# Kernel tuning notes

Measured on AMD Instinct MI355X. Metric: run time of the kernel, lower is better.

## Reference

```python
import jax, jax.numpy as jnp
import numpy as np
import math

B, T, S, C, H = 2, 2048, 576, 1024, 16
D = C // H
EPS = 1e-5


def _ln(x, w, b):
    m = jnp.mean(x, axis=-1, keepdims=True)
    v = jnp.mean((x - m) ** 2, axis=-1, keepdims=True)
    return (x - m) * jax.lax.rsqrt(v + EPS) * w + b


def setup_inputs() -> dict:
    key = jax.random.key(0)
    ks = jax.random.split(key, 20)
    s = 0.02
    return {
        "x": jax.random.normal(ks[0], (B, T, C), jnp.float32),
        "context": jax.random.normal(ks[1], (B, S, C), jnp.float32),
        "ln1_w": jnp.ones((C,), jnp.float32), "ln1_b": jnp.zeros((C,), jnp.float32),
        "ln2_w": jnp.ones((C,), jnp.float32), "ln2_b": jnp.zeros((C,), jnp.float32),
        "ln3_w": jnp.ones((C,), jnp.float32), "ln3_b": jnp.zeros((C,), jnp.float32),
        "attn_wqkv": jax.random.normal(ks[2], (C, 3 * C), jnp.float32) * s,
        "attn_bqkv": jnp.zeros((3 * C,), jnp.float32),
        "attn_wproj": jax.random.normal(ks[3], (C, C), jnp.float32) * s,
        "attn_bproj": jnp.zeros((C,), jnp.float32),
        "ca_wq": jax.random.normal(ks[4], (C, C), jnp.float32) * s,
        "ca_bq": jnp.zeros((C,), jnp.float32),
        "ca_wk": jax.random.normal(ks[5], (C, C), jnp.float32) * s,
        "ca_bk": jnp.zeros((C,), jnp.float32),
        "ca_wv": jax.random.normal(ks[6], (C, C), jnp.float32) * s,
        "ca_bv": jnp.zeros((C,), jnp.float32),
        "ca_wproj": jax.random.normal(ks[7], (C, C), jnp.float32) * s,
        "ca_bproj": jnp.zeros((C,), jnp.float32),
        "fc_w": jax.random.normal(ks[8], (C, 4 * C), jnp.float32) * s,
        "fc_b": jnp.zeros((4 * C,), jnp.float32),
        "proj_w": jax.random.normal(ks[9], (4 * C, C), jnp.float32) * s,
        "proj_b": jnp.zeros((C,), jnp.float32),
    }


def reference(x, context, ln1_w, ln1_b, ln2_w, ln2_b, ln3_w, ln3_b,
              attn_wqkv, attn_bqkv, attn_wproj, attn_bproj,
              ca_wq, ca_bq, ca_wk, ca_bk, ca_wv, ca_bv, ca_wproj, ca_bproj,
              fc_w, fc_b, proj_w, proj_b):
    b, t, c = x.shape
    scale = 1.0 / math.sqrt(D)

    # --- causal self-attention ---
    h = _ln(x, ln1_w, ln1_b)
    qkv = h @ attn_wqkv + attn_bqkv                       # [B,T,3C]
    q, k, v = jnp.split(qkv, 3, axis=-1)
    q = q.reshape(b, t, H, D).transpose(0, 2, 1, 3)       # [B,H,T,D]
    k = k.reshape(b, t, H, D).transpose(0, 2, 1, 3)
    v = v.reshape(b, t, H, D).transpose(0, 2, 1, 3)
    att = jnp.einsum('bhqd,bhkd->bhqk', q, k) * scale     # [B,H,T,T]
    causal = jnp.tril(jnp.ones((t, t), dtype=bool))
    att = jnp.where(causal, att, -jnp.inf)
    att = jax.nn.softmax(att, axis=-1)
    sa = jnp.einsum('bhqk,bhkd->bhqd', att, v).transpose(0, 2, 1, 3).reshape(b, t, c)
    x = x + sa @ attn_wproj + attn_bproj

    # --- cross-attention ---
    h = _ln(x, ln2_w, ln2_b)
    s = context.shape[1]
    q = (h @ ca_wq + ca_bq).reshape(b, t, H, D).transpose(0, 2, 1, 3)        # [B,H,T,D]
    k = (context @ ca_wk + ca_bk).reshape(b, s, H, D).transpose(0, 2, 1, 3)  # [B,H,S,D]
    v = (context @ ca_wv + ca_bv).reshape(b, s, H, D).transpose(0, 2, 1, 3)
    scores = jnp.einsum('bhqd,bhkd->bhqk', q, k) * scale                      # [B,H,T,S]
    attn_prob = jax.nn.softmax(scores, axis=-1)
    ca = jnp.einsum('bhqk,bhkd->bhqd', attn_prob, v).transpose(0, 2, 1, 3).reshape(b, t, c)
    x = x + ca @ ca_wproj + ca_bproj

    # --- GELU(tanh) MLP ---
    h = _ln(x, ln3_w, ln3_b)
    h = jax.nn.gelu(h @ fc_w + fc_b, approximate=True)
    x = x + h @ proj_w + proj_b
    return x, attn_prob
```

## Files before the change

kernel.cpp:

```cpp
#include <hip/hip_runtime.h>

typedef __bf16 bf16_t;
typedef __attribute__((ext_vector_type(8))) __bf16 bf16x8;
typedef __attribute__((ext_vector_type(4))) __bf16 bf16x4;
typedef __attribute__((ext_vector_type(4))) float f32x4;

static constexpr int kB = 2, kT = 2048, kS = 576, kC = 1024, kH = 16, kD = 64;

#define MFMA16(a, b, c) __builtin_amdgcn_mfma_f32_16x16x32_bf16((a), (b), (c), 0, 0, 0)

__device__ __forceinline__ void gld_lds16(const bf16_t* g, bf16_t* l) {
    __builtin_amdgcn_global_load_lds((const __attribute__((address_space(1))) unsigned int*)g,
                                     (__attribute__((address_space(3))) unsigned int*)l, 16, 0, 0);
}

__device__ __forceinline__ int swz(int row, int q) { return row * 64 + (((q ^ (row & 7)) & 7) << 3); }

__device__ inline float gelu_tanh(float x) {
    float u = 1.5957691216057308f * (x + 0.044715f * x * x * x);
    float t = 1.f - 2.f / (__expf(u) + 1.f);
    return 0.5f * x * (1.f + t);
}

__global__ void transpose_w(const float* __restrict__ W, bf16_t* __restrict__ WT, int K, int N) {
    __shared__ float tile[32][33];
    int n0 = blockIdx.x * 32, k0 = blockIdx.y * 32;
    int tx = threadIdx.x, ty = threadIdx.y;
#pragma unroll
    for (int i = 0; i < 4; ++i)
        tile[ty + i * 8][tx] = W[(size_t)(k0 + ty + i * 8) * N + n0 + tx];
    __syncthreads();
#pragma unroll
    for (int i = 0; i < 4; ++i)
        WT[(size_t)(n0 + ty + i * 8) * K + k0 + tx] = (bf16_t)tile[tx][ty + i * 8];
}

__global__ void f32_to_bf16(const float* __restrict__ in, bf16_t* __restrict__ out, int n4) {
    int i = blockIdx.x * 256 + threadIdx.x;
    if (i < n4) {
        float4 v = ((const float4*)in)[i];
        bf16x4 o;
        o[0] = (bf16_t)v.x; o[1] = (bf16_t)v.y; o[2] = (bf16_t)v.z; o[3] = (bf16_t)v.w;
        ((bf16x4*)out)[i] = o;
    }
}

__global__ __launch_bounds__(256) void ln_kernel(const float* __restrict__ x,
                                                 const float* __restrict__ w,
                                                 const float* __restrict__ bb,
                                                 bf16_t* __restrict__ out) {
    int row = blockIdx.x, tid = threadIdx.x;
    const float* xr = x + (size_t)row * kC;
    float4 v = ((const float4*)xr)[tid];
    float s1 = v.x + v.y + v.z + v.w;
    float s2 = v.x * v.x + v.y * v.y + v.z * v.z + v.w * v.w;
#pragma unroll
    for (int o = 32; o > 0; o >>= 1) {
        s1 += __shfl_down(s1, o);
        s2 += __shfl_down(s2, o);
    }
    __shared__ float red[8];
    __shared__ float mv[2];
    int wid = tid >> 6, lane = tid & 63;
    if (lane == 0) { red[wid] = s1; red[4 + wid] = s2; }
    __syncthreads();
    if (tid == 0) {
        float a = red[0] + red[1] + red[2] + red[3];
        float c = red[4] + red[5] + red[6] + red[7];
        float mean = a * (1.f / kC);
        float var = c * (1.f / kC) - mean * mean;
        mv[0] = mean;
        mv[1] = rsqrtf(var + 1e-5f);
    }
    __syncthreads();
    float mean = mv[0], rstd = mv[1];
    float4 wv = ((const float4*)w)[tid];
    float4 bv = ((const float4*)bb)[tid];
    bf16x4 o4;
    o4[0] = (bf16_t)((v.x - mean) * rstd * wv.x + bv.x);
    o4[1] = (bf16_t)((v.y - mean) * rstd * wv.y + bv.y);
    o4[2] = (bf16_t)((v.z - mean) * rstd * wv.z + bv.z);
    o4[3] = (bf16_t)((v.w - mean) * rstd * wv.w + bv.w);
    *(bf16x4*)&out[(size_t)row * kC + tid * 4] = o4;
}

#define VWAIT(n) asm volatile("s_waitcnt vmcnt(" #n ")" ::: "memory")
#define CFENCE() asm volatile("" ::: "memory")

template <int EPI, int BM>
__global__ __launch_bounds__(256) void gemm128(const bf16_t* __restrict__ A, const bf16_t* __restrict__ Bw,
                                               const float* __restrict__ bias, const float* __restrict__ res,
                                               void* __restrict__ Out, void* __restrict__ Out2,
                                               void* __restrict__ Out3, int M, int N, int K, int lda, int ldb,
                                               int ldc) {
    constexpr int MT = BM / 32;
    constexpr int ASZ = BM * 64, BSZ = 128 * 64;
    __shared__ __align__(16) bf16_t As[2 * ASZ];
    __shared__ __align__(16) bf16_t Bs[2 * BSZ];
    const int tid = threadIdx.x;
    const int m0 = blockIdx.y * BM, n0 = blockIdx.x * 128;
    const int lane = tid & 63, wid = tid >> 6;
    const int l16 = lane & 15, quad = lane >> 4;
    const int wm = (wid >> 1) * (BM / 2), wn = (wid & 1) * 64;
    f32x4 acc[MT][4] = {};

    const bf16_t* Ab = A + (size_t)m0 * lda;
    const bf16_t* Bb = Bw + (size_t)n0 * ldb;

    auto stage = [&](int buf, int k0) {
#pragma unroll
        for (int i = 0; i < BM / 32; ++i) {
            int chunk = tid + i * 256;
            int row = chunk >> 3, c8 = chunk & 7;
            gld_lds16(Ab + (size_t)row * lda + k0 + ((c8 ^ (row & 7)) << 3), As + buf * ASZ + chunk * 8);
        }
#pragma unroll
        for (int i = 0; i < 4; ++i) {
            int chunk = tid + i * 256;
            int row = chunk >> 3, c8 = chunk & 7;
            gld_lds16(Bb + (size_t)row * ldb + k0 + ((c8 ^ (row & 7)) << 3), Bs + buf * BSZ + chunk * 8);
        }
    };

    const int nk = K / 64;
    stage(0, 0);
    int cur = 0;
    for (int t = 0; t < nk; ++t) {
        __builtin_amdgcn_s_barrier();
        CFENCE();
        if (t + 1 < nk) {
            stage(cur ^ 1, (t + 1) * 64);
            if constexpr (BM == 64) VWAIT(6); else VWAIT(8);
        } else {
            VWAIT(0);
        }
        __builtin_amdgcn_s_barrier();
        CFENCE();
#pragma unroll
        for (int kk = 0; kk < 2; ++kk) {
            bf16x8 af[MT], bw[4];
#pragma unroll
            for (int mt = 0; mt < MT; ++mt)
                af[mt] = *(const bf16x8*)&As[cur * ASZ + swz(wm + mt * 16 + l16, kk * 4 + quad)];
#pragma unroll
            for (int nt = 0; nt < 4; ++nt)
                bw[nt] = *(const bf16x8*)&Bs[cur * BSZ + swz(wn + nt * 16 + l16, kk * 4 + quad)];
#pragma unroll
            for (int mt = 0; mt < MT; ++mt)
#pragma unroll
                for (int nt = 0; nt < 4; ++nt) acc[mt][nt] = MFMA16(af[mt], bw[nt], acc[mt][nt]);
        }
        cur ^= 1;
    }

#pragma unroll
    for (int mt = 0; mt < MT; ++mt)
#pragma unroll
        for (int nt = 0; nt < 4; ++nt) {
            int n = n0 + wn + nt * 16 + l16;
            float bv = bias ? bias[n] : 0.f;
#pragma unroll
            for (int r = 0; r < 4; ++r) {
                int m = m0 + wm + mt * 16 + quad * 4 + r;
                float v = acc[mt][nt][r] + bv;
                if constexpr (EPI == 2) v = gelu_tanh(v);
                if constexpr (EPI == 0 || EPI == 2) {
                    ((bf16_t*)Out)[(size_t)m * ldc + n] = (bf16_t)v;
                } else if constexpr (EPI == 1) {
                    ((float*)Out)[(size_t)m * ldc + n] = v + res[(size_t)m * ldc + n];
                } else {
                    int b = m >> 11, t = m & 2047;
                    if (n < 2048) {
                        int h = (n & 1023) >> 6, d = n & 63;
                        bf16_t* dst = (n < 1024) ? (bf16_t*)Out : (bf16_t*)Out2;
                        dst[(((size_t)b * kH + h) * kT + t) * kD + d] = (bf16_t)v;
                    } else {
                        int n2 = n - 2048;
                        int h = n2 >> 6, d = n2 & 63;
                        ((bf16_t*)Out3)[(((size_t)b * kH + h) * kD + d) * kT + t] = (bf16_t)v;
                    }
                }
            }
        }
}

__global__ __launch_bounds__(256) void flash_self4(const bf16_t* __restrict__ qb, const bf16_t* __restrict__ kb,
                                                   const bf16_t* __restrict__ vT, bf16_t* __restrict__ sa) {
    const int tid = threadIdx.x;
    const int qi = gridDim.x - 1 - blockIdx.x;
    const int h = blockIdx.y, b = blockIdx.z;
    const int lane = tid & 63, wid = tid >> 6;
    const int l16 = lane & 15, quad = lane >> 4;
    const size_t bh = (size_t)b * kH + h;
    constexpr int TSZ = 64 * 64;

    __shared__ __align__(16) bf16_t Qs[TSZ];
    __shared__ __align__(16) bf16_t Ks[2 * TSZ];
    __shared__ __align__(16) bf16_t VTs[2 * TSZ];
    bf16_t* Ps = Qs;

    const bf16_t* qsrc = qb + (bh * kT + (size_t)qi * 64) * kD;
    const bf16_t* kbase = kb + bh * kT * kD;
    const bf16_t* vbase = vT + bh * kD * kT;

#pragma unroll
    for (int i = 0; i < 2; ++i) {
        int chunk = tid + i * 256;
        int row = chunk >> 3, c8 = chunk & 7;
        gld_lds16(qsrc + row * 64 + ((c8 ^ (row & 7)) << 3), Qs + chunk * 8);
    }

    auto stageKV = [&](int buf, int kt) {
        const bf16_t* ksrc = kbase + (size_t)kt * 64 * kD;
        const bf16_t* vsrc = vbase + (size_t)kt * 64;
#pragma unroll
        for (int i = 0; i < 2; ++i) {
            int chunk = tid + i * 256;
            int row = chunk >> 3, c8 = chunk & 7;
            int sc = (c8 ^ (row & 7)) << 3;
            gld_lds16(ksrc + row * 64 + sc, Ks + buf * TSZ + chunk * 8);
            gld_lds16(vsrc + (size_t)row * kT + sc, VTs + buf * TSZ + chunk * 8);
        }
    };
    stageKV(0, 0);

    __syncthreads();
    bf16x8 aq[2];
    aq[0] = *(const bf16x8*)&Qs[swz(wid * 16 + l16, quad)];
    aq[1] = *(const bf16x8*)&Qs[swz(wid * 16 + l16, 4 + quad)];
#pragma unroll
    for (int j = 0; j < 8; ++j) { aq[0][j] *= (bf16_t)0.125f; aq[1][j] *= (bf16_t)0.125f; }

    f32x4 o[4] = {};
    float lsum[4] = {0.f, 0.f, 0.f, 0.f};
    const int qrow = qi * 64 + wid * 16 + quad * 4;
    int cur = 0;

    for (int kt = 0; kt <= qi; ++kt) {
        if (kt) __syncthreads();
        if (kt < qi) stageKV(cur ^ 1, kt + 1);

        f32x4 sf[4] = {};
#pragma unroll
        for (int kk = 0; kk < 2; ++kk)
#pragma unroll
            for (int nt = 0; nt < 4; ++nt) {
                bf16x8 bk = *(const bf16x8*)&Ks[cur * TSZ + swz(nt * 16 + l16, kk * 4 + quad)];
                sf[nt] = MFMA16(aq[kk], bk, sf[nt]);
            }

        const bool diag = (kt == qi);
#pragma unroll
        for (int nt = 0; nt < 4; ++nt) {
            int col = kt * 64 + nt * 16 + l16;
#pragma unroll
            for (int r = 0; r < 4; ++r) {
                float s = sf[nt][r];
                if (diag && col > qrow + r) s = -1e30f;
                float p = __expf(s);
                lsum[r] += p;
                int rp = wid * 16 + quad * 4 + r;
                int cc = nt * 16 + l16;
                Ps[rp * 64 + (cc ^ ((rp & 7) << 3))] = (bf16_t)p;
            }
        }
#pragma unroll
        for (int kk = 0; kk < 2; ++kk) {
            bf16x8 ap = *(const bf16x8*)&Ps[swz(wid * 16 + l16, kk * 4 + quad)];
#pragma unroll
            for (int dt = 0; dt < 4; ++dt) {
                bf16x8 bv = *(const bf16x8*)&VTs[cur * TSZ + swz(dt * 16 + l16, kk * 4 + quad)];
                o[dt] = MFMA16(ap, bv, o[dt]);
            }
        }
        cur ^= 1;
    }

#pragma unroll
    for (int r = 0; r < 4; ++r) {
        float s = lsum[r];
#pragma unroll
        for (int off = 1; off < 16; off <<= 1) s += __shfl_xor(s, off, 16);
        float inv = 1.f / s;
        size_t row = (size_t)b * kT + qi * 64 + wid * 16 + quad * 4 + r;
#pragma unroll
        for (int dt = 0; dt < 4; ++dt)
            sa[row * kC + h * kD + dt * 16 + l16] = (bf16_t)(o[dt][r] * inv);
    }
}

__global__ __launch_bounds__(256) void ca_fused(const bf16_t* __restrict__ q2, const bf16_t* __restrict__ k2,
                                                const bf16_t* __restrict__ v2T, bf16_t* __restrict__ ca,
                                                float* __restrict__ probs) {
    const int tid = threadIdx.x;
    const int qi = blockIdx.x, z = blockIdx.y;
    const int b = z >> 4, h = z & 15;
    const int lane = tid & 63, wid = tid >> 6;
    const int l16 = lane & 15, quad = lane >> 4;
    const size_t bh = (size_t)z;
    constexpr int TSZ = 64 * 64;

    __shared__ __align__(16) bf16_t Qs[TSZ];
    __shared__ __align__(16) bf16_t Ks[2 * TSZ];
    __shared__ __align__(16) bf16_t VTs[2 * TSZ];
    bf16_t* Ps = Qs;

#pragma unroll
    for (int i = 0; i < 2; ++i) {
        int chunk = tid + i * 256;
        int row = chunk >> 3, c8 = chunk & 7;
        gld_lds16(q2 + ((size_t)(b * kT + qi * 64 + row)) * kC + h * kD + ((c8 ^ (row & 7)) << 3),
                  Qs + chunk * 8);
    }

    auto stageKV = [&](int buf, int kt) {
#pragma unroll
        for (int i = 0; i < 2; ++i) {
            int chunk = tid + i * 256;
            int row = chunk >> 3, c8 = chunk & 7;
            int sc = (c8 ^ (row & 7)) << 3;
            gld_lds16(k2 + ((size_t)(b * kS + kt * 64 + row)) * kC + h * kD + sc, Ks + buf * TSZ + chunk * 8);
            gld_lds16(v2T + (bh * kD + row) * kS + kt * 64 + sc, VTs + buf * TSZ + chunk * 8);
        }
    };
    stageKV(0, 0);

    __syncthreads();
    bf16x8 aq[2];
    aq[0] = *(const bf16x8*)&Qs[swz(wid * 16 + l16, quad)];
    aq[1] = *(const bf16x8*)&Qs[swz(wid * 16 + l16, 4 + quad)];
#pragma unroll
    for (int j = 0; j < 8; ++j) { aq[0][j] *= (bf16_t)0.125f; aq[1][j] *= (bf16_t)0.125f; }

    f32x4 o[4] = {};
    float lsum[4] = {0.f, 0.f, 0.f, 0.f};
    bf16x4 pk[9][4];
    int cur = 0;

#pragma unroll
    for (int kt = 0; kt < 9; ++kt) {
        if (kt) __syncthreads();
        if (kt < 8) stageKV(cur ^ 1, kt + 1);

        f32x4 sf[4] = {};
#pragma unroll
        for (int kk = 0; kk < 2; ++kk)
#pragma unroll
            for (int nt = 0; nt < 4; ++nt) {
                bf16x8 bk = *(const bf16x8*)&Ks[cur * TSZ + swz(nt * 16 + l16, kk * 4 + quad)];
                sf[nt] = MFMA16(aq[kk], bk, sf[nt]);
            }
#pragma unroll
        for (int nt = 0; nt < 4; ++nt) {
            bf16x4 pc;
#pragma unroll
            for (int r = 0; r < 4; ++r) {
                float p = __expf(sf[nt][r]);
                lsum[r] += p;
                bf16_t pb = (bf16_t)p;
                pc[r] = pb;
                int rp = wid * 16 + quad * 4 + r;
                int cc = nt * 16 + l16;
                Ps[rp * 64 + (cc ^ ((rp & 7) << 3))] = pb;
            }
            pk[kt][nt] = pc;
        }
#pragma unroll
        for (int kk = 0; kk < 2; ++kk) {
            bf16x8 ap = *(const bf16x8*)&Ps[swz(wid * 16 + l16, kk * 4 + quad)];
#pragma unroll
            for (int dt = 0; dt < 4; ++dt) {
                bf16x8 bv = *(const bf16x8*)&VTs[cur * TSZ + swz(dt * 16 + l16, kk * 4 + quad)];
                o[dt] = MFMA16(ap, bv, o[dt]);
            }
        }
        cur ^= 1;
    }

    float inv[4];
#pragma unroll
    for (int r = 0; r < 4; ++r) {
        float s = lsum[r];
#pragma unroll
        for (int off = 1; off < 16; off <<= 1) s += __shfl_xor(s, off, 16);
        inv[r] = 1.f / s;
        size_t row = (size_t)b * kT + qi * 64 + wid * 16 + quad * 4 + r;
#pragma unroll
        for (int dt = 0; dt < 4; ++dt)
            ca[row * kC + h * kD + dt * 16 + l16] = (bf16_t)(o[dt][r] * inv[r]);
    }
#pragma unroll
    for (int r = 0; r < 4; ++r) {
        float* dst = probs + ((size_t)z * kT + qi * 64 + wid * 16 + quad * 4 + r) * kS;
#pragma unroll
        for (int kt = 0; kt < 9; ++kt)
#pragma unroll
            for (int nt = 0; nt < 4; ++nt)
                dst[kt * 64 + nt * 16 + l16] = (float)pk[kt][nt][r] * inv[r];
    }
}

__global__ void v_transpose(const bf16_t* __restrict__ v2, bf16_t* __restrict__ v2T) {
    int idx = blockIdx.x * 256 + threadIdx.x;
    int s = idx % kS;
    int t = idx / kS;
    int d = t % kD; t /= kD;
    int h = t % kH;
    int b = t / kH;
    v2T[idx] = v2[((size_t)(b * kS + s)) * kC + h * kD + d];
}

extern "C" void kernel_launch(void* const* d_in, const int* in_sizes, int n_in, void* d_out, int out_size,
                              void* d_ws, size_t ws_size, hipStream_t stream) {
    const float* x = (const float*)d_in[0];
    const float* context = (const float*)d_in[1];
    const float* ln1_w = (const float*)d_in[2];
    const float* ln1_b = (const float*)d_in[3];
    const float* ln2_w = (const float*)d_in[4];
    const float* ln2_b = (const float*)d_in[5];
    const float* ln3_w = (const float*)d_in[6];
    const float* ln3_b = (const float*)d_in[7];
    const float* attn_wqkv = (const float*)d_in[8];
    const float* attn_bqkv = (const float*)d_in[9];
    const float* attn_wproj = (const float*)d_in[10];
    const float* attn_bproj = (const float*)d_in[11];
    const float* ca_wq = (const float*)d_in[12];
    const float* ca_bq = (const float*)d_in[13];
    const float* ca_wk = (const float*)d_in[14];
    const float* ca_bk = (const float*)d_in[15];
    const float* ca_wv = (const float*)d_in[16];
    const float* ca_bv = (const float*)d_in[17];
    const float* ca_wproj = (const float*)d_in[18];
    const float* ca_bproj = (const float*)d_in[19];
    const float* fc_w = (const float*)d_in[20];
    const float* fc_b = (const float*)d_in[21];
    const float* proj_w = (const float*)d_in[22];
    const float* proj_b = (const float*)d_in[23];

    float* out_x = (float*)d_out;
    float* probs = out_x + (size_t)kB * kT * kC;

    char* wsp = (char*)d_ws;
    size_t off = 0;
    auto alloc = [&](size_t bytes) -> void* {
        void* p = wsp + off;
        off += (bytes + 255) & ~(size_t)255;
        return p;
    };
    bf16_t* wT_qkv   = (bf16_t*)alloc((size_t)3 * kC * kC * 2);
    bf16_t* wT_aproj = (bf16_t*)alloc((size_t)kC * kC * 2);
    bf16_t* wT_caq   = (bf16_t*)alloc((size_t)kC * kC * 2);
    bf16_t* wT_cak   = (bf16_t*)alloc((size_t)kC * kC * 2);
    bf16_t* wT_cav   = (bf16_t*)alloc((size_t)kC * kC * 2);
    bf16_t* wT_caproj= (bf16_t*)alloc((size_t)kC * kC * 2);
    bf16_t* wT_fc    = (bf16_t*)alloc((size_t)4 * kC * kC * 2);
    bf16_t* wT_proj  = (bf16_t*)alloc((size_t)4 * kC * kC * 2);
    bf16_t* hbuf     = (bf16_t*)alloc((size_t)kB * kT * kC * 2);
    bf16_t* qb       = (bf16_t*)alloc((size_t)kB * kT * kC * 2);
    bf16_t* kbuf     = (bf16_t*)alloc((size_t)kB * kT * kC * 2);
    bf16_t* vTb      = (bf16_t*)alloc((size_t)kB * kT * kC * 2);
    bf16_t* sabuf    = (bf16_t*)alloc((size_t)kB * kT * kC * 2);
    float*  x1       = (float*)alloc((size_t)kB * kT * kC * 4);
    float*  x2       = (float*)alloc((size_t)kB * kT * kC * 4);
    bf16_t* ctxb     = (bf16_t*)alloc((size_t)kB * kS * kC * 2);
    bf16_t* q2       = (bf16_t*)alloc((size_t)kB * kT * kC * 2);
    bf16_t* k2       = (bf16_t*)alloc((size_t)kB * kS * kC * 2);
    bf16_t* v2       = (bf16_t*)alloc((size_t)kB * kS * kC * 2);
    bf16_t* v2T      = (bf16_t*)alloc((size_t)kB * kS * kC * 2);
    bf16_t* hf       = (bf16_t*)alloc((size_t)kB * kT * 4 * kC * 2);
    (void)ws_size;

    dim3 tb(32, 8);
    transpose_w<<<dim3(96, 32), tb, 0, stream>>>(attn_wqkv, wT_qkv, kC, 3 * kC);
    transpose_w<<<dim3(32, 32), tb, 0, stream>>>(attn_wproj, wT_aproj, kC, kC);
    transpose_w<<<dim3(32, 32), tb, 0, stream>>>(ca_wq, wT_caq, kC, kC);
    transpose_w<<<dim3(32, 32), tb, 0, stream>>>(ca_wk, wT_cak, kC, kC);
    transpose_w<<<dim3(32, 32), tb, 0, stream>>>(ca_wv, wT_cav, kC, kC);
    transpose_w<<<dim3(32, 32), tb, 0, stream>>>(ca_wproj, wT_caproj, kC, kC);
    transpose_w<<<dim3(128, 32), tb, 0, stream>>>(fc_w, wT_fc, kC, 4 * kC);
    transpose_w<<<dim3(32, 128), tb, 0, stream>>>(proj_w, wT_proj, 4 * kC, kC);
    f32_to_bf16<<<dim3((kB * kS * kC / 4 + 255) / 256), 256, 0, stream>>>(context, ctxb, kB * kS * kC / 4);

    const int Mtok = kB * kT;
    ln_kernel<<<Mtok, 256, 0, stream>>>(x, ln1_w, ln1_b, hbuf);
    gemm128<4, 128><<<dim3(24, 32), 256, 0, stream>>>(hbuf, wT_qkv, attn_bqkv, nullptr, qb, kbuf, vTb, Mtok,
                                                      3 * kC, kC, kC, kC, 0);
    flash_self4<<<dim3(kT / 64, kH, kB), 256, 0, stream>>>(qb, kbuf, vTb, sabuf);
    gemm128<1, 64><<<dim3(8, 64), 256, 0, stream>>>(sabuf, wT_aproj, attn_bproj, x, x1, nullptr, nullptr, Mtok,
                                                    kC, kC, kC, kC, kC);
    ln_kernel<<<Mtok, 256, 0, stream>>>(x1, ln2_w, ln2_b, hbuf);
    gemm128<0, 64><<<dim3(8, 64), 256, 0, stream>>>(hbuf, wT_caq, ca_bq, nullptr, q2, nullptr, nullptr, Mtok, kC,
                                                    kC, kC, kC, kC);
    gemm128<0, 64><<<dim3(8, 18), 256, 0, stream>>>(ctxb, wT_cak, ca_bk, nullptr, k2, nullptr, nullptr, kB * kS,
                                                    kC, kC, kC, kC, kC);
    gemm128<0, 64><<<dim3(8, 18), 256, 0, stream>>>(ctxb, wT_cav, ca_bv, nullptr, v2, nullptr, nullptr, kB * kS,
                                                    kC, kC, kC, kC, kC);
    v_transpose<<<dim3(kB * kH * kD * kS / 256), 256, 0, stream>>>(v2, v2T);
    ca_fused<<<dim3(kT / 64, kB * kH), 256, 0, stream>>>(q2, k2, v2T, sabuf, probs);
    gemm128<1, 64><<<dim3(8, 64), 256, 0, stream>>>(sabuf, wT_caproj, ca_bproj, x1, x2, nullptr, nullptr, Mtok,
                                                    kC, kC, kC, kC, kC);
    ln_kernel<<<Mtok, 256, 0, stream>>>(x2, ln3_w, ln3_b, hbuf);
    gemm128<2, 128><<<dim3(32, 32), 256, 0, stream>>>(hbuf, wT_fc, fc_b, nullptr, hf, nullptr, nullptr, Mtok,
                                                      4 * kC, kC, kC, kC, 4 * kC);
    gemm128<1, 64><<<dim3(8, 64), 256, 0, stream>>>(hf, wT_proj, proj_b, x2, out_x, nullptr, nullptr, Mtok, kC,
                                                    4 * kC, 4 * kC, 4 * kC, kC);
}
```

Baseline: 706.8 us.

## Batch weight prep, fuse cross-attn K/V GEMM, widen flash tiles, swizzle GEMM blocks

Measured after the change: 682.1 us. 1.04x faster.

```diff
diff --git a/kernel.cpp b/kernel.cpp
--- a/kernel.cpp
+++ b/kernel.cpp
@@ -22,10 +22,13 @@
     return 0.5f * x * (1.f + t);
 }
 
-__global__ void transpose_w(const float* __restrict__ W, bf16_t* __restrict__ WT, int K, int N) {
-    __shared__ float tile[32][33];
-    int n0 = blockIdx.x * 32, k0 = blockIdx.y * 32;
-    int tx = threadIdx.x, ty = threadIdx.y;
+#define VWAIT(n) asm volatile("s_waitcnt vmcnt(" #n ")" ::: "memory")
+#define CFENCE() asm volatile("" ::: "memory")
+
+__device__ __forceinline__ void do_tr(float (*tile)[33], const float* __restrict__ W, bf16_t* __restrict__ WT,
+                                      int K, int N, int t, int nx, int tid) {
+    int n0 = (t % nx) * 32, k0 = (t / nx) * 32;
+    int tx = tid & 31, ty = tid >> 5;
 #pragma unroll
     for (int i = 0; i < 4; ++i)
         tile[ty + i * 8][tx] = W[(size_t)(k0 + ty + i * 8) * N + n0 + tx];
@@ -35,13 +38,34 @@
         WT[(size_t)(n0 + ty + i * 8) * K + k0 + tx] = (bf16_t)tile[tx][ty + i * 8];
 }
 
-__global__ void f32_to_bf16(const float* __restrict__ in, bf16_t* __restrict__ out, int n4) {
-    int i = blockIdx.x * 256 + threadIdx.x;
-    if (i < n4) {
-        float4 v = ((const float4*)in)[i];
-        bf16x4 o;
-        o[0] = (bf16_t)v.x; o[1] = (bf16_t)v.y; o[2] = (bf16_t)v.z; o[3] = (bf16_t)v.w;
-        ((bf16x4*)out)[i] = o;
+__global__ __launch_bounds__(256) void batch_prep(const float* __restrict__ w_qkv, const float* __restrict__ w_aproj,
+                                                  const float* __restrict__ w_caq, const float* __restrict__ w_cak,
+                                                  const float* __restrict__ w_cav, const float* __restrict__ w_caproj,
+                                                  const float* __restrict__ w_fc, const float* __restrict__ w_proj,
+                                                  const float* __restrict__ ctx,
+                                                  bf16_t* __restrict__ wT_qkv, bf16_t* __restrict__ wT_aproj,
+                                                  bf16_t* __restrict__ wT_caq, bf16_t* __restrict__ wT_cakv,
+                                                  bf16_t* __restrict__ wT_caproj, bf16_t* __restrict__ wT_fc,
+                                                  bf16_t* __restrict__ wT_proj, bf16_t* __restrict__ ctxb) {
+    __shared__ float tile[32][33];
+    int bid = blockIdx.x, tid = threadIdx.x;
+    if (bid < 3072)        do_tr(tile, w_qkv, wT_qkv, 1024, 3072, bid, 96, tid);
+    else if (bid < 4096)   do_tr(tile, w_aproj, wT_aproj, 1024, 1024, bid - 3072, 32, tid);
+    else if (bid < 5120)   do_tr(tile, w_caq, wT_caq, 1024, 1024, bid - 4096, 32, tid);
+    else if (bid < 6144)   do_tr(tile, w_cak, wT_cakv, 1024, 1024, bid - 5120, 32, tid);
+    else if (bid < 7168)   do_tr(tile, w_cav, wT_cakv + (size_t)1024 * 1024, 1024, 1024, bid - 6144, 32, tid);
+    else if (bid < 8192)   do_tr(tile, w_caproj, wT_caproj, 1024, 1024, bid - 7168, 32, tid);
+    else if (bid < 12288)  do_tr(tile, w_fc, wT_fc, 1024, 4096, bid - 8192, 128, tid);
+    else if (bid < 16384)  do_tr(tile, w_proj, wT_proj, 4096, 1024, bid - 12288, 32, tid);
+    else {
+        int i = (bid - 16384) * 256 + tid;
+        const int n4 = kB * kS * kC / 4;
+        if (i < n4) {
+            float4 v = ((const float4*)ctx)[i];
+            bf16x4 o;
+            o[0] = (bf16_t)v.x; o[1] = (bf16_t)v.y; o[2] = (bf16_t)v.z; o[3] = (bf16_t)v.w;
+            ((bf16x4*)ctxb)[i] = o;
+        }
     }
 }
 
@@ -84,9 +108,6 @@
     *(bf16x4*)&out[(size_t)row * kC + tid * 4] = o4;
 }
 
-#define VWAIT(n) asm volatile("s_waitcnt vmcnt(" #n ")" ::: "memory")
-#define CFENCE() asm volatile("" ::: "memory")
-
 template <int EPI, int BM>
 __global__ __launch_bounds__(256) void gemm128(const bf16_t* __restrict__ A, const bf16_t* __restrict__ Bw,
                                                const float* __restrict__ bias, const float* __restrict__ res,
@@ -98,7 +119,10 @@
     __shared__ __align__(16) bf16_t As[2 * ASZ];
     __shared__ __align__(16) bf16_t Bs[2 * BSZ];
     const int tid = threadIdx.x;
-    const int m0 = blockIdx.y * BM, n0 = blockIdx.x * 128;
+    const int nwg = gridDim.x * gridDim.y;
+    const int orig = blockIdx.y * gridDim.x + blockIdx.x;
+    const int wg = (orig & 7) * (nwg >> 3) + (orig >> 3);
+    const int m0 = (wg / gridDim.x) * BM, n0 = (wg % gridDim.x) * 128;
     const int lane = tid & 63, wid = tid >> 6;
     const int l16 = lane & 15, quad = lane >> 4;
     const int wm = (wid >> 1) * (BM / 2), wn = (wid & 1) * 64;
@@ -136,6 +160,7 @@
         }
         __builtin_amdgcn_s_barrier();
         CFENCE();
+        __builtin_amdgcn_s_setprio(1);
 #pragma unroll
         for (int kk = 0; kk < 2; ++kk) {
             bf16x8 af[MT], bw[4];
@@ -150,6 +175,7 @@
 #pragma unroll
                 for (int nt = 0; nt < 4; ++nt) acc[mt][nt] = MFMA16(af[mt], bw[nt], acc[mt][nt]);
         }
+        __builtin_amdgcn_s_setprio(0);
         cur ^= 1;
     }
 
@@ -158,7 +184,9 @@
 #pragma unroll
         for (int nt = 0; nt < 4; ++nt) {
             int n = n0 + wn + nt * 16 + l16;
-            float bv = bias ? bias[n] : 0.f;
+            float bv;
+            if constexpr (EPI == 5) bv = (n < kC) ? bias[n] : res[n - kC];
+            else bv = bias ? bias[n] : 0.f;
 #pragma unroll
             for (int r = 0; r < 4; ++r) {
                 int m = m0 + wm + mt * 16 + quad * 4 + r;
@@ -168,6 +196,15 @@
                     ((bf16_t*)Out)[(size_t)m * ldc + n] = (bf16_t)v;
                 } else if constexpr (EPI == 1) {
                     ((float*)Out)[(size_t)m * ldc + n] = v + res[(size_t)m * ldc + n];
+                } else if constexpr (EPI == 5) {
+                    int b2 = (m >= kS) ? 1 : 0;
+                    int s2 = m - b2 * kS;
+                    if (n < kC) {
+                        ((bf16_t*)Out)[(size_t)m * kC + n] = (bf16_t)v;
+                    } else {
+                        int n2 = n - kC, hh = n2 >> 6, d = n2 & 63;
+                        ((bf16_t*)Out2)[(((size_t)b2 * kH + hh) * kD + d) * kS + s2] = (bf16_t)v;
+                    }
                 } else {
                     int b = m >> 11, t = m & 2047;
                     if (n < 2048) {
@@ -184,7 +221,7 @@
         }
 }
 
-__global__ __launch_bounds__(256) void flash_self4(const bf16_t* __restrict__ qb, const bf16_t* __restrict__ kb,
+__global__ __launch_bounds__(256) void flash_self5(const bf16_t* __restrict__ qb, const bf16_t* __restrict__ kb,
                                                    const bf16_t* __restrict__ vT, bf16_t* __restrict__ sa) {
     const int tid = threadIdx.x;
     const int qi = gridDim.x - 1 - blockIdx.x;
@@ -194,25 +231,25 @@
     const size_t bh = (size_t)b * kH + h;
     constexpr int TSZ = 64 * 64;
 
-    __shared__ __align__(16) bf16_t Qs[TSZ];
+    __shared__ __align__(16) bf16_t Qs[2 * TSZ];
     __shared__ __align__(16) bf16_t Ks[2 * TSZ];
     __shared__ __align__(16) bf16_t VTs[2 * TSZ];
     bf16_t* Ps = Qs;
 
-    const bf16_t* qsrc = qb + (bh * kT + (size_t)qi * 64) * kD;
+    const bf16_t* qsrc = qb + (bh * kT + (size_t)qi * 128) * kD;
     const bf16_t* kbase = kb + bh * kT * kD;
     const bf16_t* vbase = vT + bh * kD * kT;
 
 #pragma unroll
-    for (int i = 0; i < 2; ++i) {
+    for (int i = 0; i < 4; ++i) {
         int chunk = tid + i * 256;
         int row = chunk >> 3, c8 = chunk & 7;
         gld_lds16(qsrc + row * 64 + ((c8 ^ (row & 7)) << 3), Qs + chunk * 8);
     }
 
-    auto stageKV = [&](int buf, int kt) {
-        const bf16_t* ksrc = kbase + (size_t)kt * 64 * kD;
-        const bf16_t* vsrc = vbase + (size_t)kt * 64;
+    auto stageKV = [&](int buf, int kt2) {
+        const bf16_t* ksrc = kbase + (size_t)kt2 * 64 * kD;
+        const bf16_t* vsrc = vbase + (size_t)kt2 * 64;
 #pragma unroll
         for (int i = 0; i < 2; ++i) {
             int chunk = tid + i * 256;
@@ -223,70 +260,87 @@
         }
     };
     stageKV(0, 0);
-
-    __syncthreads();
-    bf16x8 aq[2];
-    aq[0] = *(const bf16x8*)&Qs[swz(wid * 16 + l16, quad)];
-    aq[1] = *(const bf16x8*)&Qs[swz(wid * 16 + l16, 4 + quad)];
-#pragma unroll
-    for (int j = 0; j < 8; ++j) { aq[0][j] *= (bf16_t)0.125f; aq[1][j] *= (bf16_t)0.125f; }
-
-    f32x4 o[4] = {};
-    float lsum[4] = {0.f, 0.f, 0.f, 0.f};
-    const int qrow = qi * 64 + wid * 16 + quad * 4;
+    VWAIT(4);
+    __builtin_amdgcn_s_barrier();
+    CFENCE();
+
+    bf16x8 aq[2][2];
+#pragma unroll
+    for (int u = 0; u < 2; ++u) {
+        int row = u * 64 + wid * 16 + l16;
+        aq[u][0] = *(const bf16x8*)&Qs[swz(row, quad)];
+        aq[u][1] = *(const bf16x8*)&Qs[swz(row, 4 + quad)];
+#pragma unroll
+        for (int j = 0; j < 8; ++j) { aq[u][0][j] *= (bf16_t)0.125f; aq[u][1][j] *= (bf16_t)0.125f; }
+    }
+
+    f32x4 o[2][4] = {};
+    float lsum[2][4] = {};
     int cur = 0;
-
-    for (int kt = 0; kt <= qi; ++kt) {
-        if (kt) __syncthreads();
-        if (kt < qi) stageKV(cur ^ 1, kt + 1);
-
-        f32x4 sf[4] = {};
-#pragma unroll
-        for (int kk = 0; kk < 2; ++kk)
+    const int nkt = 2 * qi + 2;
+
+    for (int kt = 0; kt < nkt; ++kt) {
+        __builtin_amdgcn_s_barrier();
+        CFENCE();
+        if (kt + 1 < nkt) { stageKV(cur ^ 1, kt + 1); VWAIT(4); }
+        else VWAIT(0);
+        __builtin_amdgcn_s_barrier();
+        CFENCE();
+
+        const bool skip0 = (kt == 2 * qi + 1);
+#pragma unroll
+        for (int u = 0; u < 2; ++u) {
+            if (u == 0 && skip0) continue;
+            f32x4 sf[4] = {};
+#pragma unroll
+            for (int kk = 0; kk < 2; ++kk)
+#pragma unroll
+                for (int nt = 0; nt < 4; ++nt) {
+                    bf16x8 bk = *(const bf16x8*)&Ks[cur * TSZ + swz(nt * 16 + l16, kk * 4 + quad)];
+                    sf[nt] = MFMA16(aq[u][kk], bk, sf[nt]);
+                }
+            const bool diag = (kt == 2 * qi + u);
+            const int qrow = qi * 128 + u * 64 + wid * 16 + quad * 4;
 #pragma unroll
             for (int nt = 0; nt < 4; ++nt) {
-                bf16x8 bk = *(const bf16x8*)&Ks[cur * TSZ + swz(nt * 16 + l16, kk * 4 + quad)];
-                sf[nt] = MFMA16(aq[kk], bk, sf[nt]);
+                int col = kt * 64 + nt * 16 + l16;
+#pragma unroll
+                for (int r = 0; r < 4; ++r) {
+                    float s = sf[nt][r];
+                    if (diag && col > qrow + r) s = -1e30f;
+                    float p = __expf(s);
+                    lsum[u][r] += p;
+                    int rp = wid * 16 + quad * 4 + r;
+                    int cc = nt * 16 + l16;
+                    Ps[u * TSZ + rp * 64 + (cc ^ ((rp & 7) << 3))] = (bf16_t)p;
+                }
             }
-
-        const bool diag = (kt == qi);
-#pragma unroll
-        for (int nt = 0; nt < 4; ++nt) {
-            int col = kt * 64 + nt * 16 + l16;
-#pragma unroll
-            for (int r = 0; r < 4; ++r) {
-                float s = sf[nt][r];
-                if (diag && col > qrow + r) s = -1e30f;
-                float p = __expf(s);
-                lsum[r] += p;
-                int rp = wid * 16 + quad * 4 + r;
-                int cc = nt * 16 + l16;
-                Ps[rp * 64 + (cc ^ ((rp & 7) << 3))] = (bf16_t)p;
+#pragma unroll
+            for (int kk = 0; kk < 2; ++kk) {
+                bf16x8 ap = *(const bf16x8*)&Ps[u * TSZ + swz(wid * 16 + l16, kk * 4 + quad)];
+#pragma unroll
+                for (int dt = 0; dt < 4; ++dt) {
+                    bf16x8 bv = *(const bf16x8*)&VTs[cur * TSZ + swz(dt * 16 + l16, kk * 4 + quad)];
+                    o[u][dt] = MFMA16(ap, bv, o[u][dt]);
+                }
             }
         }
-#pragma unroll
-        for (int kk = 0; kk < 2; ++kk) {
-            bf16x8 ap = *(const bf16x8*)&Ps[swz(wid * 16 + l16, kk * 4 + quad)];
-#pragma unroll
-            for (int dt = 0; dt < 4; ++dt) {
-                bf16x8 bv = *(const bf16x8*)&VTs[cur * TSZ + swz(dt * 16 + l16, kk * 4 + quad)];
-                o[dt] = MFMA16(ap, bv, o[dt]);
-            }
-        }
         cur ^= 1;
     }
 
 #pragma unroll
-    for (int r = 0; r < 4; ++r) {
-        float s = lsum[r];
-#pragma unroll
-        for (int off = 1; off < 16; off <<= 1) s += __shfl_xor(s, off, 16);
-        float inv = 1.f / s;
-        size_t row = (size_t)b * kT + qi * 64 + wid * 16 + quad * 4 + r;
-#pragma unroll
-        for (int dt = 0; dt < 4; ++dt)
-            sa[row * kC + h * kD + dt * 16 + l16] = (bf16_t)(o[dt][r] * inv);
-    }
+    for (int u = 0; u < 2; ++u)
+#pragma unroll
+        for (int r = 0; r < 4; ++r) {
+            float s = lsum[u][r];
+#pragma unroll
+            for (int off = 1; off < 16; off <<= 1) s += __shfl_xor(s, off, 16);
+            float inv = 1.f / s;
+            size_t row = (size_t)b * kT + qi * 128 + u * 64 + wid * 16 + quad * 4 + r;
+#pragma unroll
+            for (int dt = 0; dt < 4; ++dt)
+                sa[row * kC + h * kD + dt * 16 + l16] = (bf16_t)(o[u][dt][r] * inv);
+        }
 }
 
 __global__ __launch_bounds__(256) void ca_fused(const bf16_t* __restrict__ q2, const bf16_t* __restrict__ k2,
@@ -324,8 +378,10 @@
         }
     };
     stageKV(0, 0);
-
-    __syncthreads();
+    VWAIT(4);
+    __builtin_amdgcn_s_barrier();
+    CFENCE();
+
     bf16x8 aq[2];
     aq[0] = *(const bf16x8*)&Qs[swz(wid * 16 + l16, quad)];
     aq[1] = *(const bf16x8*)&Qs[swz(wid * 16 + l16, 4 + quad)];
@@ -339,8 +395,12 @@
 
 #pragma unroll
     for (int kt = 0; kt < 9; ++kt) {
-        if (kt) __syncthreads();
-        if (kt < 8) stageKV(cur ^ 1, kt + 1);
+        __builtin_amdgcn_s_barrier();
+        CFENCE();
+        if (kt < 8) { stageKV(cur ^ 1, kt + 1); VWAIT(4); }
+        else VWAIT(0);
+        __builtin_amdgcn_s_barrier();
+        CFENCE();
 
         f32x4 sf[4] = {};
 #pragma unroll
@@ -398,16 +458,6 @@
             for (int nt = 0; nt < 4; ++nt)
                 dst[kt * 64 + nt * 16 + l16] = (float)pk[kt][nt][r] * inv[r];
     }
-}
-
-__global__ void v_transpose(const bf16_t* __restrict__ v2, bf16_t* __restrict__ v2T) {
-    int idx = blockIdx.x * 256 + threadIdx.x;
-    int s = idx % kS;
-    int t = idx / kS;
-    int d = t % kD; t /= kD;
-    int h = t % kH;
-    int b = t / kH;
-    v2T[idx] = v2[((size_t)(b * kS + s)) * kC + h * kD + d];
 }
 
 extern "C" void kernel_launch(void* const* d_in, const int* in_sizes, int n_in, void* d_out, int out_size,
@@ -450,8 +500,7 @@
     bf16_t* wT_qkv   = (bf16_t*)alloc((size_t)3 * kC * kC * 2);
     bf16_t* wT_aproj = (bf16_t*)alloc((size_t)kC * kC * 2);
     bf16_t* wT_caq   = (bf16_t*)alloc((size_t)kC * kC * 2);
-    bf16_t* wT_cak   = (bf16_t*)alloc((size_t)kC * kC * 2);
-    bf16_t* wT_cav   = (bf16_t*)alloc((size_t)kC * kC * 2);
+    bf16_t* wT_cakv  = (bf16_t*)alloc((size_t)2 * kC * kC * 2);
     bf16_t* wT_caproj= (bf16_t*)alloc((size_t)kC * kC * 2);
     bf16_t* wT_fc    = (bf16_t*)alloc((size_t)4 * kC * kC * 2);
     bf16_t* wT_proj  = (bf16_t*)alloc((size_t)4 * kC * kC * 2);
@@ -465,37 +514,26 @@
     bf16_t* ctxb     = (bf16_t*)alloc((size_t)kB * kS * kC * 2);
     bf16_t* q2       = (bf16_t*)alloc((size_t)kB * kT * kC * 2);
     bf16_t* k2       = (bf16_t*)alloc((size_t)kB * kS * kC * 2);
-    bf16_t* v2       = (bf16_t*)alloc((size_t)kB * kS * kC * 2);
     bf16_t* v2T      = (bf16_t*)alloc((size_t)kB * kS * kC * 2);
     bf16_t* hf       = (bf16_t*)alloc((size_t)kB * kT * 4 * kC * 2);
     (void)ws_size;
 
-    dim3 tb(32, 8);
-    transpose_w<<<dim3(96, 32), tb, 0, stream>>>(attn_wqkv, wT_qkv, kC, 3 * kC);
-    transpose_w<<<dim3(32, 32), tb, 0, stream>>>(attn_wproj, wT_aproj, kC, kC);
-    transpose_w<<<dim3(32, 32), tb, 0, stream>>>(ca_wq, wT_caq, kC, kC);
-    transpose_w<<<dim3(32, 32), tb, 0, stream>>>(ca_wk, wT_cak, kC, kC);
-    transpose_w<<<dim3(32, 32), tb, 0, stream>>>(ca_wv, wT_cav, kC, kC);
-    transpose_w<<<dim3(32, 32), tb, 0, stream>>>(ca_wproj, wT_caproj, kC, kC);
-    transpose_w<<<dim3(128, 32), tb, 0, stream>>>(fc_w, wT_fc, kC, 4 * kC);
-    transpose_w<<<dim3(32, 128), tb, 0, stream>>>(proj_w, wT_proj, 4 * kC, kC);
-    f32_to_bf16<<<dim3((kB * kS * kC / 4 + 255) / 256), 256, 0, stream>>>(context, ctxb, kB * kS * kC / 4);
+    batch_prep<<<dim3(17536), 256, 0, stream>>>(attn_wqkv, attn_wproj, ca_wq, ca_wk, ca_wv, ca_wproj, fc_w,
+                                                proj_w, context, wT_qkv, wT_aproj, wT_caq, wT_cakv, wT_caproj,
+                                                wT_fc, wT_proj, ctxb);
 
     const int Mtok = kB * kT;
     ln_kernel<<<Mtok, 256, 0, stream>>>(x, ln1_w, ln1_b, hbuf);
     gemm128<4, 128><<<dim3(24, 32), 256, 0, stream>>>(hbuf, wT_qkv, attn_bqkv, nullptr, qb, kbuf, vTb, Mtok,
                                                       3 * kC, kC, kC, kC, 0);
-    flash_self4<<<dim3(kT / 64, kH, kB), 256, 0, stream>>>(qb, kbuf, vTb, sabuf);
+    flash_self5<<<dim3(kT / 128, kH, kB), 256, 0, stream>>>(qb, kbuf, vTb, sabuf);
     gemm128<1, 64><<<dim3(8, 64), 256, 0, stream>>>(sabuf, wT_aproj, attn_bproj, x, x1, nullptr, nullptr, Mtok,
                                                     kC, kC, kC, kC, kC);
     ln_kernel<<<Mtok, 256, 0, stream>>>(x1, ln2_w, ln2_b, hbuf);
     gemm128<0, 64><<<dim3(8, 64), 256, 0, stream>>>(hbuf, wT_caq, ca_bq, nullptr, q2, nullptr, nullptr, Mtok, kC,
                                                     kC, kC, kC, kC);
-    gemm128<0, 64><<<dim3(8, 18), 256, 0, stream>>>(ctxb, wT_cak, ca_bk, nullptr, k2, nullptr, nullptr, kB * kS,
-                                                    kC, kC, kC, kC, kC);
-    gemm128<0, 64><<<dim3(8, 18), 256, 0, stream>>>(ctxb, wT_cav, ca_bv, nullptr, v2, nullptr, nullptr, kB * kS,
-                                                    kC, kC, kC, kC, kC);
-    v_transpose<<<dim3(kB * kH * kD * kS / 256), 256, 0, stream>>>(v2, v2T);
+    gemm128<5, 64><<<dim3(16, 18), 256, 0, stream>>>(ctxb, wT_cakv, ca_bk, ca_bv, k2, v2T, nullptr, kB * kS,
+                                                     2 * kC, kC, kC, kC, 0);
     ca_fused<<<dim3(kT / 64, kB * kH), 256, 0, stream>>>(q2, k2, v2T, sabuf, probs);
     gemm128<1, 64><<<dim3(8, 64), 256, 0, stream>>>(sabuf, wT_caproj, ca_bproj, x1, x2, nullptr, nullptr, Mtok,
                                                     kC, kC, kC, kC, kC);
```
